# Performance work log

Hardware: AMD Instinct MI355X
Metric: run time of the kernel (lower is better)

The kernel has to match this reference:

```python
import jax, jax.numpy as jnp
import numpy as np

N_DYADIC = 0  # dyadic refinement order n (init kwarg)


def _solve_pde(inc):
    """Solve the signature-kernel Goursat PDE by finite differences.

    inc: (A, Mi, Ni) inner products <dx_i, dy_j> on the (refined) grid.
    Recurrence on grid K of shape (Mi+1, Ni+1):
      K[0,:] = K[:,0] = 1
      K[i,j] = K[i,j-1] + K[i-1,j] + K[i-1,j-1] * (inc[i-1,j-1] - 1)
    Implemented as an anti-diagonal wavefront (vectorized over batch and
    along each diagonal) so there is no O(M*N) sequential loop.
    Returns K[:, -1, -1], shape (A,).
    """
    A, Mi, Ni = inc.shape
    P = Mi + 1                      # number of grid rows
    ivec = jnp.arange(P)            # row index along a diagonal
    n_diags = Mi + Ni + 1           # diagonals d = i + j in [0, Mi+Ni]

    def step(carry, d):
        prev, prev2 = carry         # diagonals d-1 and d-2, shape (A, P)
        j = d - ivec                # column index for each row on diag d
        inc_d = inc[:, jnp.clip(ivec - 1, 0, Mi - 1),
                       jnp.clip(j - 1, 0, Ni - 1)]          # (A, P)
        # K[i,j-1] = prev[i]; K[i-1,j] = prev[i-1]; K[i-1,j-1] = prev2[i-1]
        interior = prev + jnp.roll(prev, 1, axis=1) \
                 + jnp.roll(prev2, 1, axis=1) * (inc_d - 1.0)
        in_grid = (j >= 0) & (j <= Ni)
        boundary = (ivec == 0) | (j == 0)
        new = jnp.where(in_grid, jnp.where(boundary, 1.0, interior), 0.0)
        return (new, prev), None

    init = (jnp.zeros((A, P), inc.dtype), jnp.zeros((A, P), inc.dtype))
    (last, _), _ = jax.lax.scan(step, init, jnp.arange(n_diags))
    return last[:, Mi]              # K at grid point (Mi, Ni)


def _sig_kernel(X, Y, n):
    """k(x_a, y_a) for each pair in the batch, via PDE solve."""
    f = 2 ** n
    dX = X[:, 1:] - X[:, :-1]                          # (A, M-1, D)
    dY = Y[:, 1:] - Y[:, :-1]                          # (A, N-1, D)
    C = jnp.einsum('amd,and->amn', dX, dY)             # (A, M-1, N-1)
    # dyadic refinement: each coarse increment split into 2^n equal pieces
    inc = jnp.repeat(jnp.repeat(C, f, axis=1), f, axis=2) / float(f * f)
    return _solve_pde(inc)


def setup_inputs() -> dict:
    key = jax.random.key(0)
    kx, ky = jax.random.split(key)
    A, M, D = 128, 512, 16
    # small-increment random walks so the signature kernel stays bounded
    X = 0.05 * jnp.cumsum(jax.random.normal(kx, (A, M, D), dtype=jnp.float32), axis=1)
    Y = 0.05 * jnp.cumsum(jax.random.normal(ky, (A, M, D), dtype=jnp.float32), axis=1)
    return {"X": X, "Y": Y}


def reference(X, Y):
    # SigLoss: mean_a [ k(x,x) + k(y,y) - 2 k(x,y) ]
    k_xx = _sig_kernel(X, X, N_DYADIC)
    k_yy = _sig_kernel(Y, Y, N_DYADIC)
    k_xy = _sig_kernel(X, Y, N_DYADIC)
    return jnp.mean(k_xx + k_yy - 2.0 * k_xy)
```

## Files before the change

kernel.cpp:

```cpp
#include <hip/hip_runtime.h>

#define D 16

typedef short bf16x8 __attribute__((ext_vector_type(8)));
typedef float f32x16 __attribute__((ext_vector_type(16)));
typedef float v2f __attribute__((ext_vector_type(2)));

template<int CTRL, int RMASK, bool BC>
__device__ __forceinline__ float dpp_add(float x) {
    int t = __builtin_amdgcn_update_dpp(0, __float_as_int(x), CTRL, RMASK, 0xF, BC);
    return x + __int_as_float(t);
}
__device__ __forceinline__ float wave_iscan(float x) {
    x = dpp_add<0x111, 0xF, true >(x);
    x = dpp_add<0x112, 0xF, true >(x);
    x = dpp_add<0x114, 0xF, true >(x);
    x = dpp_add<0x118, 0xF, true >(x);
    x = dpp_add<0x142, 0xA, false>(x);
    x = dpp_add<0x143, 0xC, false>(x);
    return x;
}

__device__ __forceinline__ short f2bf(float f) {
    unsigned u = __float_as_uint(f);
    unsigned r = u + 0x7FFFu + ((u >> 16) & 1u);
    return (short)(r >> 16);
}

__global__ __launch_bounds__(64, 1)
void sig_pde_kernel(const float* __restrict__ X, const float* __restrict__ Y,
                    float* __restrict__ out) {
    __shared__ float sinc[32 * 512];

    const int idx  = blockIdx.x;
    const int pair = idx >> 7;
    const int a    = idx & 127;
    const float* Pp = (pair == 1) ? Y : X;
    const float* Qp = (pair == 0) ? X : Y;
    const float* prow = Pp + (size_t)a * 512 * D;
    const float* qrow = Qp + (size_t)a * 512 * D;

    const int l  = threadIdx.x;
    const int lm = l & 31;
    const int kh = l >> 5;
    const int d0 = kh * 8;
    const bool lane0 = (l == 0);

    bf16x8 Bf[16];
    #pragma unroll
    for (int n = 0; n < 16; ++n) {
        int jj = 32 * n + lm - 1;
        if (jj < 0) jj = 0;
        const float4* y1 = (const float4*)(qrow + (size_t)(jj + 1) * D + d0);
        const float4* y0 = (const float4*)(qrow + (size_t)jj * D + d0);
        float4 h1 = y1[0], h0 = y0[0], g1 = y1[1], g0 = y0[1];
        bf16x8 f;
        f[0] = f2bf(h1.x - h0.x); f[1] = f2bf(h1.y - h0.y);
        f[2] = f2bf(h1.z - h0.z); f[3] = f2bf(h1.w - h0.w);
        f[4] = f2bf(g1.x - g0.x); f[5] = f2bf(g1.y - g0.y);
        f[6] = f2bf(g1.z - g0.z); f[7] = f2bf(g1.w - g0.w);
        Bf[n] = f;
    }

    auto loadA = [&](int b) -> bf16x8 {
        int ii = 32 * b + lm - 1;
        if (ii < 0) ii = 0;
        const float4* x1 = (const float4*)(prow + (size_t)(ii + 1) * D + d0);
        const float4* x0 = (const float4*)(prow + (size_t)ii * D + d0);
        float4 h1 = x1[0], h0 = x0[0], g1 = x1[1], g0 = x0[1];
        bf16x8 f;
        f[0] = f2bf(h1.x - h0.x); f[1] = f2bf(h1.y - h0.y);
        f[2] = f2bf(h1.z - h0.z); f[3] = f2bf(h1.w - h0.w);
        f[4] = f2bf(g1.x - g0.x); f[5] = f2bf(g1.y - g0.y);
        f[6] = f2bf(g1.z - g0.z); f[7] = f2bf(g1.w - g0.w);
        return f;
    };

    const int rot = (l >> 2) & 7;
    float* wbase = sinc + kh * 2048;

    int ea4[8];
    #pragma unroll
    for (int m = 0; m < 8; ++m) ea4[m] = (8 * l + ((m + rot) & 7)) * 4;

    float s[8];
    #pragma unroll
    for (int m = 0; m < 8; ++m) s[m] = 0.0f;
    float B = 1.0f;

    v2f ghA[8], ghB[8];
    float eA[8], eB[8];

    const f32x16 accC = {-1.f,-1.f,-1.f,-1.f,-1.f,-1.f,-1.f,-1.f,
                         -1.f,-1.f,-1.f,-1.f,-1.f,-1.f,-1.f,-1.f};

#define PREF(BUF, RB) do {                                                    \
        const char* pb_ = (const char*)sinc + (RB);                           \
        _Pragma("unroll")                                                     \
        for (int m_ = 0; m_ < 8; ++m_)                                        \
            BUF[m_] = *(const float*)(pb_ + ea4[m_]);                         \
    } while (0)

#define TOUCH(BUF) do { float tt_ = BUF[7];                                   \
        asm volatile("" : "+v"(tt_)); BUF[7] = tt_; } while (0)

#define GHBUILD(GH, E) do {                                                   \
        float p0_ = E[0] + 1.0f;  p0_ = lane0 ? 0.0f : p0_;                   \
        float c0_ = lane0 ? 0.0f : s[0];                                      \
        GH[0][0] = p0_; GH[0][1] = c0_;                                       \
        _Pragma("unroll")                                                     \
        for (int m_ = 1; m_ < 8; ++m_) {                                      \
            v2f pc_;                                                          \
            pc_[0] = E[m_] + 1.0f;                                            \
            pc_[1] = fmaf(s[m_ - 1], E[m_], s[m_]);                          \
            GH[m_] = GH[m_ - 1] + pc_;                                        \
        }                                                                     \
    } while (0)

#define SFMA(GH) do {                                                         \
        _Pragma("unroll")                                                     \
        for (int m_ = 0; m_ < 8; ++m_)                                        \
            s[m_] = fmaf(B, GH[m_][0], GH[m_][1]);                            \
    } while (0)

#define STEPROW(GHC, EP, RP, EN, GHN) do {                                    \
        TOUCH(EN);                                                            \
        SFMA(GHC);                                                            \
        float S_ = s[7];                                                      \
        float W_ = wave_iscan(S_);                      \
        PREF(EP, RP);                                     \
        GHBUILD(GHN, EN);                     \
        B = 1.0f + (W_ - S_);                                                 \
    } while (0)

#define TAILROW(GHC) do {                                                     \
        SFMA(GHC);                                                            \
        float S_ = s[7];                                                      \
        float W_ = wave_iscan(S_);                                            \
        B = 1.0f + (W_ - S_);                                                 \
    } while (0)

    bf16x8 Acur = loadA(0);

    for (int b = 0; b < 16; ++b) {
        #pragma unroll
        for (int n = 0; n < 16; ++n) {
            f32x16 acc = __builtin_amdgcn_mfma_f32_32x32x16_bf16(Acur, Bf[n], accC, 0, 0, 0);
            float* p = wbase + 32 * n + (lm & ~7) + (((l & 7) + n) & 7);
            #pragma unroll
            for (int r = 0; r < 16; ++r)
                p[(r & 3) * 512 + (r >> 2) * 4096] = acc[r];
        }
        if (b < 15) Acur = loadA(b + 1);

        if (b == 0) {
            #pragma unroll
            for (int m = 0; m < 8; ++m) { ghA[m][0] = 0.0f; ghA[m][1] = 0.0f; }
            PREF(eB, 2048);
        } else {
            PREF(eA, 0);
            PREF(eB, 2048);
            GHBUILD(ghA, eA);
        }
        for (int i = 0; i < 15; ++i) {
            const int rp1 = (2 * i + 2) * 2048;
            const int rp2 = (2 * i + 3) * 2048;
            STEPROW(ghA, eA, rp1, eB, ghB);
            STEPROW(ghB, eB, rp2, eA, ghA);
        }
        STEPROW(ghA, eA, 31 * 2048, eB, ghB);
        TAILROW(ghB);
    }

#undef TAILROW
#undef STEPROW
#undef SFMA
#undef GHBUILD
#undef TOUCH
#undef PREF

    if (l == 63) out[idx] = B + s[7];
}

__global__ void sig_reduce_kernel(const float* __restrict__ ws,
                                  float* __restrict__ out) {
    const int a = threadIdx.x;
    float v = ws[a] + ws[128 + a] - 2.0f * ws[256 + a];
    #pragma unroll
    for (int off = 32; off >= 1; off >>= 1) v += __shfl_down(v, off, 64);
    __shared__ float partial[2];
    if ((a & 63) == 0) partial[a >> 6] = v;
    __syncthreads();
    if (a == 0) out[0] = (partial[0] + partial[1]) * (1.0f / 128.0f);
}

extern "C" void kernel_launch(void* const* d_in, const int* in_sizes, int n_in,
                              void* d_out, int out_size, void* d_ws, size_t ws_size,
                              hipStream_t stream) {
    const float* X = (const float*)d_in[0];
    const float* Y = (const float*)d_in[1];
    float* out = (float*)d_out;
    float* ws  = (float*)d_ws;

    sig_pde_kernel<<<dim3(384), dim3(64), 0, stream>>>(X, Y, ws);
    sig_reduce_kernel<<<dim3(1), dim3(128), 0, stream>>>(ws, out);
}
```

Baseline: 93.19 us.

## Interleave two PDE problems per wavefront and split GEMM/scan into half-tiles

Each workgroup now solves two batch pairs at once. Their MFMA increment tiles and wavefront scan steps are interleaved, so the two independent DPP scan and FMA chains can hide each other's latency. The 32-row LDS tile is split into two 16-row halves per problem, alternating GEMM and scan phases. The grid is halved to 192 blocks, which lowers CU-level parallelism and raises register pressure in exchange for more instruction-level parallelism inside each wave.

Result: slower. 200.2 us (+114.8%).

```diff
diff --git a/kernel.cpp b/kernel.cpp
--- a/kernel.cpp
+++ b/kernel.cpp
@@ -5,21 +5,6 @@
 typedef short bf16x8 __attribute__((ext_vector_type(8)));
 typedef float f32x16 __attribute__((ext_vector_type(16)));
 typedef float v2f __attribute__((ext_vector_type(2)));
-
-template<int CTRL, int RMASK, bool BC>
-__device__ __forceinline__ float dpp_add(float x) {
-    int t = __builtin_amdgcn_update_dpp(0, __float_as_int(x), CTRL, RMASK, 0xF, BC);
-    return x + __int_as_float(t);
-}
-__device__ __forceinline__ float wave_iscan(float x) {
-    x = dpp_add<0x111, 0xF, true >(x);
-    x = dpp_add<0x112, 0xF, true >(x);
-    x = dpp_add<0x114, 0xF, true >(x);
-    x = dpp_add<0x118, 0xF, true >(x);
-    x = dpp_add<0x142, 0xA, false>(x);
-    x = dpp_add<0x143, 0xC, false>(x);
-    return x;
-}
 
 __device__ __forceinline__ short f2bf(float f) {
     unsigned u = __float_as_uint(f);
@@ -30,39 +15,60 @@
 __global__ __launch_bounds__(64, 1)
 void sig_pde_kernel(const float* __restrict__ X, const float* __restrict__ Y,
                     float* __restrict__ out) {
-    __shared__ float sinc[32 * 512];
-
-    const int idx  = blockIdx.x;
-    const int pair = idx >> 7;
-    const int a    = idx & 127;
-    const float* Pp = (pair == 1) ? Y : X;
-    const float* Qp = (pair == 0) ? X : Y;
-    const float* prow = Pp + (size_t)a * 512 * D;
-    const float* qrow = Qp + (size_t)a * 512 * D;
+    __shared__ float sinc[2 * 16 * 512];
+
+    const int bid  = blockIdx.x;
+    const int idx0 = 2 * bid;
+    const int idx1 = idx0 + 1;
+
+    const int pair0 = idx0 >> 7, a0 = idx0 & 127;
+    const int pair1 = idx1 >> 7, a1 = idx1 & 127;
+    const float* prow0 = ((pair0 == 1) ? Y : X) + (size_t)a0 * 512 * D;
+    const float* qrow0 = ((pair0 == 0) ? X : Y) + (size_t)a0 * 512 * D;
+    const float* prow1 = ((pair1 == 1) ? Y : X) + (size_t)a1 * 512 * D;
+    const float* qrow1 = ((pair1 == 0) ? X : Y) + (size_t)a1 * 512 * D;
+
+    float* lds0 = sinc;
+    float* lds1 = sinc + 16 * 512;
 
     const int l  = threadIdx.x;
     const int lm = l & 31;
     const int kh = l >> 5;
     const int d0 = kh * 8;
+    const int l7 = l & 7;
     const bool lane0 = (l == 0);
-
-    bf16x8 Bf[16];
+    const int rot = (l >> 2) & 7;
+
+    bf16x8 Bf0[16], Bf1[16];
     #pragma unroll
     for (int n = 0; n < 16; ++n) {
         int jj = 32 * n + lm - 1;
         if (jj < 0) jj = 0;
-        const float4* y1 = (const float4*)(qrow + (size_t)(jj + 1) * D + d0);
-        const float4* y0 = (const float4*)(qrow + (size_t)jj * D + d0);
-        float4 h1 = y1[0], h0 = y0[0], g1 = y1[1], g0 = y0[1];
-        bf16x8 f;
-        f[0] = f2bf(h1.x - h0.x); f[1] = f2bf(h1.y - h0.y);
-        f[2] = f2bf(h1.z - h0.z); f[3] = f2bf(h1.w - h0.w);
-        f[4] = f2bf(g1.x - g0.x); f[5] = f2bf(g1.y - g0.y);
-        f[6] = f2bf(g1.z - g0.z); f[7] = f2bf(g1.w - g0.w);
-        Bf[n] = f;
+        {
+            const float4* y1 = (const float4*)(qrow0 + (size_t)(jj + 1) * D + d0);
+            const float4* y0 = (const float4*)(qrow0 + (size_t)jj * D + d0);
+            float4 h1 = y1[0], h0 = y0[0], g1 = y1[1], g0 = y0[1];
+            bf16x8 f;
+            f[0] = f2bf(h1.x - h0.x); f[1] = f2bf(h1.y - h0.y);
+            f[2] = f2bf(h1.z - h0.z); f[3] = f2bf(h1.w - h0.w);
+            f[4] = f2bf(g1.x - g0.x); f[5] = f2bf(g1.y - g0.y);
+            f[6] = f2bf(g1.z - g0.z); f[7] = f2bf(g1.w - g0.w);
+            Bf0[n] = f;
+        }
+        {
+            const float4* y1 = (const float4*)(qrow1 + (size_t)(jj + 1) * D + d0);
+            const float4* y0 = (const float4*)(qrow1 + (size_t)jj * D + d0);
+            float4 h1 = y1[0], h0 = y0[0], g1 = y1[1], g0 = y0[1];
+            bf16x8 f;
+            f[0] = f2bf(h1.x - h0.x); f[1] = f2bf(h1.y - h0.y);
+            f[2] = f2bf(h1.z - h0.z); f[3] = f2bf(h1.w - h0.w);
+            f[4] = f2bf(g1.x - g0.x); f[5] = f2bf(g1.y - g0.y);
+            f[6] = f2bf(g1.z - g0.z); f[7] = f2bf(g1.w - g0.w);
+            Bf1[n] = f;
+        }
     }
 
-    auto loadA = [&](int b) -> bf16x8 {
+    auto loadA = [&](const float* prow, int b) -> bf16x8 {
         int ii = 32 * b + lm - 1;
         if (ii < 0) ii = 0;
         const float4* x1 = (const float4*)(prow + (size_t)(ii + 1) * D + d0);
@@ -76,26 +82,25 @@
         return f;
     };
 
-    const int rot = (l >> 2) & 7;
-    float* wbase = sinc + kh * 2048;
-
     int ea4[8];
     #pragma unroll
     for (int m = 0; m < 8; ++m) ea4[m] = (8 * l + ((m + rot) & 7)) * 4;
 
-    float s[8];
-    #pragma unroll
-    for (int m = 0; m < 8; ++m) s[m] = 0.0f;
-    float B = 1.0f;
-
-    v2f ghA[8], ghB[8];
-    float eA[8], eB[8];
+    float* wb0 = lds0 + kh * 2048 + (lm & ~7);
+    float* wb1 = lds1 + kh * 2048 + (lm & ~7);
+
+    float s0[8], s1[8];
+    #pragma unroll
+    for (int m = 0; m < 8; ++m) { s0[m] = 0.0f; s1[m] = 0.0f; }
+    float B0 = 1.0f, B1 = 1.0f;
+    v2f gh0[8], gh1[8];
+    float eA0[8], eB0[8], eA1[8], eB1[8];
 
     const f32x16 accC = {-1.f,-1.f,-1.f,-1.f,-1.f,-1.f,-1.f,-1.f,
                          -1.f,-1.f,-1.f,-1.f,-1.f,-1.f,-1.f,-1.f};
 
-#define PREF(BUF, RB) do {                                                    \
-        const char* pb_ = (const char*)sinc + (RB);                           \
+#define PREF1(BUF, LDSP, RB) do {                                             \
+        const char* pb_ = (const char*)(LDSP) + (RB);                         \
         _Pragma("unroll")                                                     \
         for (int m_ = 0; m_ < 8; ++m_)                                        \
             BUF[m_] = *(const float*)(pb_ + ea4[m_]);                         \
@@ -104,82 +109,117 @@
 #define TOUCH(BUF) do { float tt_ = BUF[7];                                   \
         asm volatile("" : "+v"(tt_)); BUF[7] = tt_; } while (0)
 
-#define GHBUILD(GH, E) do {                                                   \
-        float p0_ = E[0] + 1.0f;  p0_ = lane0 ? 0.0f : p0_;                   \
-        float c0_ = lane0 ? 0.0f : s[0];                                      \
-        GH[0][0] = p0_; GH[0][1] = c0_;                                       \
+#define GHBUILD1(GH, S, E) do {                                               \
+        float gp_ = E[0] + 1.0f;  gp_ = lane0 ? 0.0f : gp_;                   \
+        float gc_ = lane0 ? 0.0f : S[0];                                      \
+        GH[0][0] = gp_; GH[0][1] = gc_;                                       \
         _Pragma("unroll")                                                     \
         for (int m_ = 1; m_ < 8; ++m_) {                                      \
             v2f pc_;                                                          \
             pc_[0] = E[m_] + 1.0f;                                            \
-            pc_[1] = fmaf(s[m_ - 1], E[m_], s[m_]);                          \
+            pc_[1] = fmaf(S[m_ - 1], E[m_], S[m_]);                          \
             GH[m_] = GH[m_ - 1] + pc_;                                        \
         }                                                                     \
     } while (0)
 
-#define SFMA(GH) do {                                                         \
+#define SFMA1(S, BB, GH) do {                                                 \
         _Pragma("unroll")                                                     \
         for (int m_ = 0; m_ < 8; ++m_)                                        \
-            s[m_] = fmaf(B, GH[m_][0], GH[m_][1]);                            \
-    } while (0)
-
-#define STEPROW(GHC, EP, RP, EN, GHN) do {                                    \
-        TOUCH(EN);                                                            \
-        SFMA(GHC);                                                            \
-        float S_ = s[7];                                                      \
-        float W_ = wave_iscan(S_);                      \
-        PREF(EP, RP);                                     \
-        GHBUILD(GHN, EN);                     \
-        B = 1.0f + (W_ - S_);                                                 \
-    } while (0)
-
-#define TAILROW(GHC) do {                                                     \
-        SFMA(GHC);                                                            \
-        float S_ = s[7];                                                      \
-        float W_ = wave_iscan(S_);                                            \
-        B = 1.0f + (W_ - S_);                                                 \
-    } while (0)
-
-    bf16x8 Acur = loadA(0);
-
-    for (int b = 0; b < 16; ++b) {
-        #pragma unroll
-        for (int n = 0; n < 16; ++n) {
-            f32x16 acc = __builtin_amdgcn_mfma_f32_32x32x16_bf16(Acur, Bf[n], accC, 0, 0, 0);
-            float* p = wbase + 32 * n + (lm & ~7) + (((l & 7) + n) & 7);
-            #pragma unroll
-            for (int r = 0; r < 16; ++r)
-                p[(r & 3) * 512 + (r >> 2) * 4096] = acc[r];
-        }
-        if (b < 15) Acur = loadA(b + 1);
-
-        if (b == 0) {
-            #pragma unroll
-            for (int m = 0; m < 8; ++m) { ghA[m][0] = 0.0f; ghA[m][1] = 0.0f; }
-            PREF(eB, 2048);
-        } else {
-            PREF(eA, 0);
-            PREF(eB, 2048);
-            GHBUILD(ghA, eA);
-        }
-        for (int i = 0; i < 15; ++i) {
-            const int rp1 = (2 * i + 2) * 2048;
-            const int rp2 = (2 * i + 3) * 2048;
-            STEPROW(ghA, eA, rp1, eB, ghB);
-            STEPROW(ghB, eB, rp2, eA, ghA);
-        }
-        STEPROW(ghA, eA, 31 * 2048, eB, ghB);
-        TAILROW(ghB);
+            S[m_] = fmaf(BB, GH[m_][0], GH[m_][1]);                           \
+    } while (0)
+
+#define DPP2(X0, X1, CTRL, RM, BC) do {                                       \
+        int u0_ = __builtin_amdgcn_update_dpp(0, __float_as_int(X0), CTRL, RM, 0xF, BC); \
+        int u1_ = __builtin_amdgcn_update_dpp(0, __float_as_int(X1), CTRL, RM, 0xF, BC); \
+        X0 += __int_as_float(u0_); X1 += __int_as_float(u1_);                 \
+    } while (0)
+
+#define ISCAN2(X0, X1) do {                                                   \
+        DPP2(X0, X1, 0x111, 0xF, true);                                       \
+        DPP2(X0, X1, 0x112, 0xF, true);                                       \
+        DPP2(X0, X1, 0x114, 0xF, true);                                       \
+        DPP2(X0, X1, 0x118, 0xF, true);                                       \
+        DPP2(X0, X1, 0x142, 0xA, false);                                      \
+        DPP2(X0, X1, 0x143, 0xC, false);                                      \
+    } while (0)
+
+#define STEPROW2(EN0, EN1, EP0, EP1, RP) do {                                 \
+        TOUCH(EN0); TOUCH(EN1);                                               \
+        SFMA1(s0, B0, gh0); SFMA1(s1, B1, gh1);                               \
+        float S0_ = s0[7], S1_ = s1[7];                                       \
+        float W0_ = S0_, W1_ = S1_;                                           \
+        ISCAN2(W0_, W1_);                                                     \
+        PREF1(EP0, lds0, RP); PREF1(EP1, lds1, RP);                           \
+        GHBUILD1(gh0, s0, EN0); GHBUILD1(gh1, s1, EN1);                       \
+        B0 = 1.0f + (W0_ - S0_); B1 = 1.0f + (W1_ - S1_);                     \
+    } while (0)
+
+#define TAILROW2() do {                                                       \
+        SFMA1(s0, B0, gh0); SFMA1(s1, B1, gh1);                               \
+        float S0_ = s0[7], S1_ = s1[7];                                       \
+        float W0_ = S0_, W1_ = S1_;                                           \
+        ISCAN2(W0_, W1_);                                                     \
+        B0 = 1.0f + (W0_ - S0_); B1 = 1.0f + (W1_ - S1_);                     \
+    } while (0)
+
+#define GEMM_PHASE(H) do {                                                    \
+        _Pragma("unroll")                                                     \
+        for (int n_ = 0; n_ < 16; ++n_) {                                     \
+            f32x16 c0_ = __builtin_amdgcn_mfma_f32_32x32x16_bf16(Acur0, Bf0[n_], accC, 0, 0, 0); \
+            f32x16 c1_ = __builtin_amdgcn_mfma_f32_32x32x16_bf16(Acur1, Bf1[n_], accC, 0, 0, 0); \
+            float* q0_ = wb0 + 32 * n_ + ((l7 + n_) & 7);                     \
+            float* q1_ = wb1 + 32 * n_ + ((l7 + n_) & 7);                     \
+            _Pragma("unroll")                                                 \
+            for (int r_ = 0; r_ < 8; ++r_) {                                  \
+                const int off_ = (r_ & 3) * 512 + (r_ >> 2) * 4096;           \
+                q0_[off_] = c0_[8 * (H) + r_];                                \
+                q1_[off_] = c1_[8 * (H) + r_];                                \
+            }                                                                 \
+        }                                                                     \
+    } while (0)
+
+#define SCAN_PHASE(R0) do {                                                   \
+        PREF1(eA0, lds0, (R0) * 2048); PREF1(eA1, lds1, (R0) * 2048);         \
+        GHBUILD1(gh0, s0, eA0); GHBUILD1(gh1, s1, eA1);                       \
+        PREF1(eB0, lds0, ((R0) + 1) * 2048); PREF1(eB1, lds1, ((R0) + 1) * 2048); \
+        _Pragma("unroll")                                                     \
+        for (int r_ = (R0); r_ <= 14; ++r_) {                                 \
+            const int rp_ = (r_ + 2 <= 15 ? r_ + 2 : 15) * 2048;              \
+            if (((r_ - (R0)) & 1) == 0) STEPROW2(eB0, eB1, eA0, eA1, rp_);    \
+            else                        STEPROW2(eA0, eA1, eB0, eB1, rp_);    \
+        }                                                                     \
+        TAILROW2();                                                           \
+    } while (0)
+
+    bf16x8 Acur0 = loadA(prow0, 0);
+    bf16x8 Acur1 = loadA(prow1, 0);
+
+    GEMM_PHASE(0);
+    SCAN_PHASE(1);
+    GEMM_PHASE(1);
+    Acur0 = loadA(prow0, 1); Acur1 = loadA(prow1, 1);
+    SCAN_PHASE(0);
+
+    for (int b = 1; b < 16; ++b) {
+        GEMM_PHASE(0);
+        SCAN_PHASE(0);
+        GEMM_PHASE(1);
+        if (b < 15) { Acur0 = loadA(prow0, b + 1); Acur1 = loadA(prow1, b + 1); }
+        SCAN_PHASE(0);
     }
 
-#undef TAILROW
-#undef STEPROW
-#undef SFMA
-#undef GHBUILD
+#undef SCAN_PHASE
+#undef GEMM_PHASE
+#undef TAILROW2
+#undef STEPROW2
+#undef ISCAN2
+#undef DPP2
+#undef SFMA1
+#undef GHBUILD1
 #undef TOUCH
-#undef PREF
-
-    if (l == 63) out[idx] = B + s[7];
+#undef PREF1
+
+    if (l == 63) { out[idx0] = B0 + s0[7]; out[idx1] = B1 + s1[7]; }
 }
 
 __global__ void sig_reduce_kernel(const float* __restrict__ ws,
@@ -202,6 +242,6 @@
     float* out = (float*)d_out;
     float* ws  = (float*)d_ws;
 
-    sig_pde_kernel<<<dim3(384), dim3(64), 0, stream>>>(X, Y, ws);
+    sig_pde_kernel<<<dim3(192), dim3(64), 0, stream>>>(X, Y, ws);
     sig_reduce_kernel<<<dim3(1), dim3(128), 0, stream>>>(ws, out);
 }
```

## Interleave two PDE problems per wave with bf16 increment precompute kernel

Applied to the files above, without the earlier changes.

Adds a prep kernel that converts path increments to bf16 in a workspace buffer. A new dual kernel then processes two batch problems per 64-thread block, interleaving their dependent scan chains (paired DPP scans) to hide latency. GEMM and scan work are split into half-tile phases so the LDS footprint stays the same while two problems are handled. The trade-off is half the blocks (192 instead of 384), an extra kernel launch, and a global round-trip for the increments. The old path is kept as a fallback when the workspace is too small.

Measured after the change: 202.1 us. +116.9%, slower.

```diff
diff --git a/kernel.cpp b/kernel.cpp
--- a/kernel.cpp
+++ b/kernel.cpp
@@ -27,9 +27,214 @@
     return (short)(r >> 16);
 }
 
+__global__ void sig_prep_kernel(const float* __restrict__ X,
+                                const float* __restrict__ Y,
+                                unsigned short* __restrict__ T) {
+    const int blk = blockIdx.x;
+    const int src = blk >> 7;
+    const int a   = blk & 127;
+    const float* P = (src ? Y : X) + (size_t)a * 512 * D;
+    unsigned short* O = T + (size_t)blk * 512 * D;
+    for (int e = threadIdx.x; e < 511 * D; e += 256)
+        O[e] = (unsigned short)f2bf(P[e + D] - P[e]);
+    if (threadIdx.x < D) O[511 * D + threadIdx.x] = 0;
+}
+
 __global__ __launch_bounds__(64, 1)
-void sig_pde_kernel(const float* __restrict__ X, const float* __restrict__ Y,
-                    float* __restrict__ out) {
+void sig_pde_dual_kernel(const unsigned short* __restrict__ T,
+                         float* __restrict__ out) {
+    __shared__ float sinc[2 * 16 * 512];
+
+    const int bid  = blockIdx.x;
+    const int idx0 = 2 * bid, idx1 = idx0 + 1;
+    const int pair0 = idx0 >> 7, a0 = idx0 & 127;
+    const int pair1 = idx1 >> 7, a1 = idx1 & 127;
+
+    const unsigned short* TX = T;
+    const unsigned short* TY = T + (size_t)128 * 512 * D;
+    const unsigned short* tp0 = ((pair0 == 1) ? TY : TX) + (size_t)a0 * 512 * D;
+    const unsigned short* tq0 = ((pair0 == 0) ? TX : TY) + (size_t)a0 * 512 * D;
+    const unsigned short* tp1 = ((pair1 == 1) ? TY : TX) + (size_t)a1 * 512 * D;
+    const unsigned short* tq1 = ((pair1 == 0) ? TX : TY) + (size_t)a1 * 512 * D;
+
+    float* lds0 = sinc;
+    float* lds1 = sinc + 16 * 512;
+
+    const int l  = threadIdx.x;
+    const int lm = l & 31;
+    const int kh = l >> 5;
+    const int l7 = l & 7;
+    const bool lane0 = (l == 0);
+    const int rot = (l >> 2) & 7;
+
+    auto loadF = [&](const unsigned short* t, int r) -> bf16x8 {
+        int ii = r; if (ii < 0) ii = 0;
+        return *(const bf16x8*)(t + (size_t)ii * D + kh * 8);
+    };
+
+    int ea4[8];
+    #pragma unroll
+    for (int m = 0; m < 8; ++m) ea4[m] = (8 * l + ((m + rot) & 7)) * 4;
+
+    float* wb0 = lds0 + kh * 2048 + (lm & ~7);
+    float* wb1 = lds1 + kh * 2048 + (lm & ~7);
+
+    float s0[8], s1[8];
+    #pragma unroll
+    for (int m = 0; m < 8; ++m) { s0[m] = 0.0f; s1[m] = 0.0f; }
+    float B0 = 1.0f, B1 = 1.0f;
+    v2f gh0[8], gh1[8];
+    float eA0[8], eB0[8], eA1[8], eB1[8];
+
+    const f32x16 accC = {-1.f,-1.f,-1.f,-1.f,-1.f,-1.f,-1.f,-1.f,
+                         -1.f,-1.f,-1.f,-1.f,-1.f,-1.f,-1.f,-1.f};
+
+#define DPREF(BUF, LDSP, RB) do {                                             \
+        const char* pb_ = (const char*)(LDSP) + (RB);                         \
+        _Pragma("unroll")                                                     \
+        for (int m_ = 0; m_ < 8; ++m_)                                        \
+            BUF[m_] = *(const float*)(pb_ + ea4[m_]);                         \
+    } while (0)
+
+#define DTOUCH(BUF) do { float tt_ = BUF[7];                                  \
+        asm volatile("" : "+v"(tt_)); BUF[7] = tt_; } while (0)
+
+#define DGH(GH, S, E) do {                                                    \
+        float gp_ = E[0] + 1.0f;  gp_ = lane0 ? 0.0f : gp_;                   \
+        float gc_ = lane0 ? 0.0f : S[0];                                      \
+        GH[0][0] = gp_; GH[0][1] = gc_;                                       \
+        _Pragma("unroll")                                                     \
+        for (int m_ = 1; m_ < 8; ++m_) {                                      \
+            v2f pc_;                                                          \
+            pc_[0] = E[m_] + 1.0f;                                            \
+            pc_[1] = fmaf(S[m_ - 1], E[m_], S[m_]);                          \
+            GH[m_] = GH[m_ - 1] + pc_;                                        \
+        }                                                                     \
+    } while (0)
+
+#define DSF(S, BB, GH) do {                                                   \
+        _Pragma("unroll")                                                     \
+        for (int m_ = 0; m_ < 8; ++m_)                                        \
+            S[m_] = fmaf(BB, GH[m_][0], GH[m_][1]);                           \
+    } while (0)
+
+#define DPP2(X0, X1, CTRL, RM, BC) do {                                       \
+        int u0_ = __builtin_amdgcn_update_dpp(0, __float_as_int(X0), CTRL, RM, 0xF, BC); \
+        int u1_ = __builtin_amdgcn_update_dpp(0, __float_as_int(X1), CTRL, RM, 0xF, BC); \
+        X0 += __int_as_float(u0_); X1 += __int_as_float(u1_);                 \
+    } while (0)
+
+#define ISCAN2(X0, X1) do {                                                   \
+        DPP2(X0, X1, 0x111, 0xF, true);                                       \
+        DPP2(X0, X1, 0x112, 0xF, true);                                       \
+        DPP2(X0, X1, 0x114, 0xF, true);                                       \
+        DPP2(X0, X1, 0x118, 0xF, true);                                       \
+        DPP2(X0, X1, 0x142, 0xA, false);                                      \
+        DPP2(X0, X1, 0x143, 0xC, false);                                      \
+    } while (0)
+
+#define DSTEP(EN0, EN1, EP0, EP1, RP) do {                                    \
+        DTOUCH(EN0); DTOUCH(EN1);                                             \
+        DSF(s0, B0, gh0); DSF(s1, B1, gh1);                                   \
+        float S0_ = s0[7], S1_ = s1[7];                                       \
+        float W0_ = S0_, W1_ = S1_;                                           \
+        ISCAN2(W0_, W1_);                                                     \
+        DPREF(EP0, lds0, RP); DPREF(EP1, lds1, RP);                           \
+        DGH(gh0, s0, EN0); DGH(gh1, s1, EN1);                                 \
+        B0 = 1.0f + (W0_ - S0_); B1 = 1.0f + (W1_ - S1_);                     \
+    } while (0)
+
+#define DTAIL() do {                                                          \
+        DSF(s0, B0, gh0); DSF(s1, B1, gh1);                                   \
+        float S0_ = s0[7], S1_ = s1[7];                                       \
+        float W0_ = S0_, W1_ = S1_;                                           \
+        ISCAN2(W0_, W1_);                                                     \
+        B0 = 1.0f + (W0_ - S0_); B1 = 1.0f + (W1_ - S1_);                     \
+    } while (0)
+
+#define GB(N_, H_, F0, F1) do {                                               \
+        f32x16 c0_ = __builtin_amdgcn_mfma_f32_32x32x16_bf16(Acur0, F0, accC, 0, 0, 0); \
+        f32x16 c1_ = __builtin_amdgcn_mfma_f32_32x32x16_bf16(Acur1, F1, accC, 0, 0, 0); \
+        if ((N_) + 4 < 16) {                                                  \
+            F0 = loadF(tq0, 32 * ((N_) + 4) + lm - 1);                        \
+            F1 = loadF(tq1, 32 * ((N_) + 4) + lm - 1);                        \
+        }                                                                     \
+        float* g0_ = wb0 + 32 * (N_) + ((l7 + (N_)) & 7);                     \
+        float* g1_ = wb1 + 32 * (N_) + ((l7 + (N_)) & 7);                     \
+        _Pragma("unroll")                                                     \
+        for (int r_ = 0; r_ < 8; ++r_) {                                      \
+            const int off_ = (r_ & 3) * 512 + (r_ >> 2) * 4096;               \
+            g0_[off_] = c0_[8 * (H_) + r_];                                   \
+            g1_[off_] = c1_[8 * (H_) + r_];                                   \
+        }                                                                     \
+    } while (0)
+
+#define GEMM_PHASE(H) do {                                                    \
+        bf16x8 qa0 = loadF(tq0, lm - 1),       qa1 = loadF(tq1, lm - 1);      \
+        bf16x8 qb0 = loadF(tq0, 32 + lm - 1),  qb1 = loadF(tq1, 32 + lm - 1); \
+        bf16x8 qc0 = loadF(tq0, 64 + lm - 1),  qc1 = loadF(tq1, 64 + lm - 1); \
+        bf16x8 qd0 = loadF(tq0, 96 + lm - 1),  qd1 = loadF(tq1, 96 + lm - 1); \
+        GB( 0, H, qa0, qa1); GB( 1, H, qb0, qb1);                             \
+        GB( 2, H, qc0, qc1); GB( 3, H, qd0, qd1);                             \
+        GB( 4, H, qa0, qa1); GB( 5, H, qb0, qb1);                             \
+        GB( 6, H, qc0, qc1); GB( 7, H, qd0, qd1);                             \
+        GB( 8, H, qa0, qa1); GB( 9, H, qb0, qb1);                             \
+        GB(10, H, qc0, qc1); GB(11, H, qd0, qd1);                             \
+        GB(12, H, qa0, qa1); GB(13, H, qb0, qb1);                             \
+        GB(14, H, qc0, qc1); GB(15, H, qd0, qd1);                             \
+    } while (0)
+
+#define SCAN_PHASE(R0) do {                                                   \
+        DPREF(eA0, lds0, (R0) * 2048); DPREF(eA1, lds1, (R0) * 2048);         \
+        DGH(gh0, s0, eA0); DGH(gh1, s1, eA1);                                 \
+        DPREF(eB0, lds0, ((R0) + 1) * 2048); DPREF(eB1, lds1, ((R0) + 1) * 2048); \
+        _Pragma("unroll")                                                     \
+        for (int r_ = (R0); r_ <= 14; ++r_) {                                 \
+            const int rp_ = (r_ + 2 <= 15 ? r_ + 2 : 15) * 2048;              \
+            if (((r_ - (R0)) & 1) == 0) DSTEP(eB0, eB1, eA0, eA1, rp_);       \
+            else                        DSTEP(eA0, eA1, eB0, eB1, rp_);       \
+        }                                                                     \
+        DTAIL();                                                              \
+    } while (0)
+
+    bf16x8 Acur0 = loadF(tp0, lm - 1);
+    bf16x8 Acur1 = loadF(tp1, lm - 1);
+
+    GEMM_PHASE(0);
+    SCAN_PHASE(1);
+    GEMM_PHASE(1);
+    Acur0 = loadF(tp0, 32 + lm - 1); Acur1 = loadF(tp1, 32 + lm - 1);
+    SCAN_PHASE(0);
+
+    for (int b = 1; b < 16; ++b) {
+        GEMM_PHASE(0);
+        SCAN_PHASE(0);
+        GEMM_PHASE(1);
+        if (b < 15) {
+            Acur0 = loadF(tp0, 32 * (b + 1) + lm - 1);
+            Acur1 = loadF(tp1, 32 * (b + 1) + lm - 1);
+        }
+        SCAN_PHASE(0);
+    }
+
+#undef SCAN_PHASE
+#undef GEMM_PHASE
+#undef GB
+#undef DTAIL
+#undef DSTEP
+#undef ISCAN2
+#undef DPP2
+#undef DSF
+#undef DGH
+#undef DTOUCH
+#undef DPREF
+
+    if (l == 63) { out[idx0] = B0 + s0[7]; out[idx1] = B1 + s1[7]; }
+}
+
+__global__ __launch_bounds__(64, 1)
+void sig_pde_single_kernel(const float* __restrict__ X, const float* __restrict__ Y,
+                           float* __restrict__ out) {
     __shared__ float sinc[32 * 512];
 
     const int idx  = blockIdx.x;
@@ -127,9 +332,9 @@
         TOUCH(EN);                                                            \
         SFMA(GHC);                                                            \
         float S_ = s[7];                                                      \
-        float W_ = wave_iscan(S_);                      \
-        PREF(EP, RP);                                     \
-        GHBUILD(GHN, EN);                     \
+        float W_ = wave_iscan(S_);                                            \
+        PREF(EP, RP);                                                         \
+        GHBUILD(GHN, EN);                                                     \
         B = 1.0f + (W_ - S_);                                                 \
     } while (0)
 
@@ -200,8 +405,17 @@
     const float* X = (const float*)d_in[0];
     const float* Y = (const float*)d_in[1];
     float* out = (float*)d_out;
-    float* ws  = (float*)d_ws;
-
-    sig_pde_kernel<<<dim3(384), dim3(64), 0, stream>>>(X, Y, ws);
-    sig_reduce_kernel<<<dim3(1), dim3(128), 0, stream>>>(ws, out);
-}
+
+    const size_t TBYTES = (size_t)2 * 128 * 512 * D * 2;
+    if (ws_size >= TBYTES + 2048) {
+        unsigned short* T = (unsigned short*)d_ws;
+        float* part = (float*)((char*)d_ws + TBYTES);
+        sig_prep_kernel<<<dim3(256), dim3(256), 0, stream>>>(X, Y, T);
+        sig_pde_dual_kernel<<<dim3(192), dim3(64), 0, stream>>>(T, part);
+        sig_reduce_kernel<<<dim3(1), dim3(128), 0, stream>>>(part, out);
+    } else {
+        float* part = (float*)d_ws;
+        sig_pde_single_kernel<<<dim3(384), dim3(64), 0, stream>>>(X, Y, part);
+        sig_reduce_kernel<<<dim3(1), dim3(128), 0, stream>>>(part, out);
+    }
+}
```

## Pack two PDE problems per wave with half-wave scans and bf16 prep pass

Applied to the files above, without the earlier changes.

Adds a prep kernel that computes the bf16 path increments once into workspace. A new PDE kernel then assigns two batch problems to each 64-lane wave, each on a 32-lane half with 16 rows per lane and a 5-step half-wave DPP scan, and interleaves the MFMA tile generation of both problems with the scan. This halves the block count and raises the serial work per lane in exchange for fewer dependent scan steps and better MFMA/scan overlap. The original kernel is kept as a fallback when the workspace is too small.

Result: slower. 157.4 us (+68.9%).

```diff
diff --git a/kernel.cpp b/kernel.cpp
--- a/kernel.cpp
+++ b/kernel.cpp
@@ -20,6 +20,14 @@
     x = dpp_add<0x143, 0xC, false>(x);
     return x;
 }
+__device__ __forceinline__ float half_iscan(float x) {
+    x = dpp_add<0x111, 0xF, true >(x);
+    x = dpp_add<0x112, 0xF, true >(x);
+    x = dpp_add<0x114, 0xF, true >(x);
+    x = dpp_add<0x118, 0xF, true >(x);
+    x = dpp_add<0x142, 0xA, false>(x);
+    return x;
+}
 
 __device__ __forceinline__ short f2bf(float f) {
     unsigned u = __float_as_uint(f);
@@ -27,9 +35,173 @@
     return (short)(r >> 16);
 }
 
+__global__ void sig_prep_kernel(const float* __restrict__ X,
+                                const float* __restrict__ Y,
+                                unsigned short* __restrict__ T) {
+    const int blk = blockIdx.x;
+    const int src = blk >> 7;
+    const int a   = blk & 127;
+    const float* P = (src ? Y : X) + (size_t)a * 512 * D;
+    unsigned short* O = T + (size_t)blk * 512 * D;
+    for (int e = threadIdx.x; e < 511 * D; e += 256)
+        O[e] = (unsigned short)f2bf(P[e + D] - P[e]);
+    if (threadIdx.x < D) O[511 * D + threadIdx.x] = 0;
+}
+
 __global__ __launch_bounds__(64, 1)
-void sig_pde_kernel(const float* __restrict__ X, const float* __restrict__ Y,
-                    float* __restrict__ out) {
+void sig_pde_half2_kernel(const unsigned short* __restrict__ T,
+                          float* __restrict__ out) {
+    __shared__ float sinc[2 * 16 * 512];
+
+    const int bid  = blockIdx.x;
+    const int idx0 = 2 * bid, idx1 = idx0 + 1;
+    const int pair0 = idx0 >> 7, a0 = idx0 & 127;
+    const int pair1 = idx1 >> 7, a1 = idx1 & 127;
+
+    const unsigned short* TX = T;
+    const unsigned short* TY = T + (size_t)128 * 512 * D;
+    const unsigned short* tp0 = ((pair0 == 1) ? TY : TX) + (size_t)a0 * 512 * D;
+    const unsigned short* tq0 = ((pair0 == 0) ? TX : TY) + (size_t)a0 * 512 * D;
+    const unsigned short* tp1 = ((pair1 == 1) ? TY : TX) + (size_t)a1 * 512 * D;
+    const unsigned short* tq1 = ((pair1 == 0) ? TX : TY) + (size_t)a1 * 512 * D;
+
+    const int l  = threadIdx.x;
+    const int lm = l & 31;
+    const int kh = l >> 5;
+    const int l7 = l & 7;
+    const int q  = l & 31;
+    const bool q0 = (q == 0);
+
+    auto loadF = [&](const unsigned short* t, int r) -> bf16x8 {
+        int ii = r < 0 ? 0 : r;
+        return *(const bf16x8*)(t + (size_t)ii * D + kh * 8);
+    };
+
+    float* wb0 = sinc + kh * 2048 + (lm & ~7);
+    float* wb1 = sinc + 8192 + kh * 2048 + (lm & ~7);
+
+    unsigned ea8[8];
+    #pragma unroll
+    for (int m = 0; m < 8; ++m)
+        ea8[m] = (unsigned)(kh * 32768 + (16 * q + ((m + (q >> 1)) & 7)) * 4);
+
+    float s[16];
+    #pragma unroll
+    for (int m = 0; m < 16; ++m) s[m] = 0.0f;
+    float B = 1.0f;
+    v2f gh[16];
+    float eA[16], eB[16];
+
+    const f32x16 accC = {-1.f,-1.f,-1.f,-1.f,-1.f,-1.f,-1.f,-1.f,
+                         -1.f,-1.f,-1.f,-1.f,-1.f,-1.f,-1.f,-1.f};
+
+#define PREF(BUF, RB) do {                                                    \
+        const char* pb_ = (const char*)sinc + (RB);                           \
+        _Pragma("unroll")                                                     \
+        for (int m_ = 0; m_ < 16; ++m_)                                       \
+            BUF[m_] = *(const float*)(pb_ + ea8[m_ & 7] + (m_ & 8) * 4);      \
+    } while (0)
+
+#define TOUCH(BUF) do { float tt_ = BUF[15];                                  \
+        asm volatile("" : "+v"(tt_)); BUF[15] = tt_; } while (0)
+
+#define GH16(E) do {                                                          \
+        float gp_ = E[0] + 1.0f;  gp_ = q0 ? 0.0f : gp_;                      \
+        float gc_ = q0 ? 0.0f : s[0];                                         \
+        gh[0][0] = gp_; gh[0][1] = gc_;                                       \
+        _Pragma("unroll")                                                     \
+        for (int m_ = 1; m_ < 16; ++m_) {                                     \
+            v2f pc_;                                                          \
+            pc_[0] = E[m_] + 1.0f;                                            \
+            pc_[1] = fmaf(s[m_ - 1], E[m_], s[m_]);                          \
+            gh[m_] = gh[m_ - 1] + pc_;                                        \
+        }                                                                     \
+    } while (0)
+
+#define SF16() do {                                                           \
+        _Pragma("unroll")                                                     \
+        for (int m_ = 0; m_ < 16; ++m_)                                       \
+            s[m_] = fmaf(B, gh[m_][0], gh[m_][1]);                            \
+    } while (0)
+
+#define DSTEP(EN, EP, RP) do {                                                \
+        TOUCH(EN);                                                            \
+        SF16();                                                               \
+        float S_ = s[15];                                                     \
+        float W_ = half_iscan(S_);                                            \
+        PREF(EP, RP);                                                         \
+        GH16(EN);                                                             \
+        B = 1.0f + (W_ - S_);                                                 \
+    } while (0)
+
+#define DTAIL() do {                                                          \
+        SF16();                                                               \
+        float S_ = s[15];                                                     \
+        float W_ = half_iscan(S_);                                            \
+        B = 1.0f + (W_ - S_);                                                 \
+    } while (0)
+
+#define SCANP(R0) do {                                                        \
+        PREF(eA, (R0) * 2048);                                                \
+        GH16(eA);                                                             \
+        PREF(eB, ((R0) + 1) * 2048);                                          \
+        _Pragma("unroll")                                                     \
+        for (int r_ = (R0); r_ <= 14; ++r_) {                                 \
+            const int rp_ = (r_ + 2 <= 15 ? r_ + 2 : 15) * 2048;              \
+            if (((r_ - (R0)) & 1) == 0) DSTEP(eB, eA, rp_);                   \
+            else                        DSTEP(eA, eB, rp_);                   \
+        }                                                                     \
+        DTAIL();                                                              \
+    } while (0)
+
+#define GEMMP(TQ, ACUR, WB, H) do {                                           \
+        bf16x8 F_[4];                                                         \
+        _Pragma("unroll")                                                     \
+        for (int n_ = 0; n_ < 4; ++n_) F_[n_] = loadF(TQ, 32 * n_ + lm - 1);  \
+        _Pragma("unroll")                                                     \
+        for (int n_ = 0; n_ < 16; ++n_) {                                     \
+            f32x16 c_ = __builtin_amdgcn_mfma_f32_32x32x16_bf16(ACUR, F_[n_ & 3], accC, 0, 0, 0); \
+            if (n_ + 4 < 16) F_[n_ & 3] = loadF(TQ, 32 * (n_ + 4) + lm - 1);  \
+            float* g_ = (WB) + 32 * n_ + ((l7 + n_) & 7);                     \
+            _Pragma("unroll")                                                 \
+            for (int r_ = 0; r_ < 8; ++r_)                                    \
+                g_[(r_ & 3) * 512 + (r_ >> 2) * 4096] = c_[8 * (H) + r_];     \
+        }                                                                     \
+    } while (0)
+
+    bf16x8 Ac0 = loadF(tp0, lm - 1);
+    bf16x8 Ac1 = loadF(tp1, lm - 1);
+
+    for (int b = 0; b < 16; ++b) {
+        GEMMP(tq0, Ac0, wb0, 0);
+        GEMMP(tq1, Ac1, wb1, 0);
+        if (b == 0) SCANP(1);
+        else        SCANP(0);
+        GEMMP(tq0, Ac0, wb0, 1);
+        GEMMP(tq1, Ac1, wb1, 1);
+        if (b < 15) {
+            Ac0 = loadF(tp0, 32 * (b + 1) + lm - 1);
+            Ac1 = loadF(tp1, 32 * (b + 1) + lm - 1);
+        }
+        SCANP(0);
+    }
+
+#undef GEMMP
+#undef SCANP
+#undef DTAIL
+#undef DSTEP
+#undef SF16
+#undef GH16
+#undef TOUCH
+#undef PREF
+
+    if (l == 31) out[idx0] = B + s[15];
+    if (l == 63) out[idx1] = B + s[15];
+}
+
+__global__ __launch_bounds__(64, 1)
+void sig_pde_single_kernel(const float* __restrict__ X, const float* __restrict__ Y,
+                           float* __restrict__ out) {
     __shared__ float sinc[32 * 512];
 
     const int idx  = blockIdx.x;
@@ -127,9 +299,9 @@
         TOUCH(EN);                                                            \
         SFMA(GHC);                                                            \
         float S_ = s[7];                                                      \
-        float W_ = wave_iscan(S_);                      \
-        PREF(EP, RP);                                     \
-        GHBUILD(GHN, EN);                     \
+        float W_ = wave_iscan(S_);                                            \
+        PREF(EP, RP);                                                         \
+        GHBUILD(GHN, EN);                                                     \
         B = 1.0f + (W_ - S_);                                                 \
     } while (0)
 
@@ -200,8 +372,17 @@
     const float* X = (const float*)d_in[0];
     const float* Y = (const float*)d_in[1];
     float* out = (float*)d_out;
-    float* ws  = (float*)d_ws;
-
-    sig_pde_kernel<<<dim3(384), dim3(64), 0, stream>>>(X, Y, ws);
-    sig_reduce_kernel<<<dim3(1), dim3(128), 0, stream>>>(ws, out);
-}
+
+    const size_t TBYTES = (size_t)2 * 128 * 512 * D * 2;
+    if (ws_size >= TBYTES + 2048) {
+        unsigned short* T = (unsigned short*)d_ws;
+        float* part = (float*)((char*)d_ws + TBYTES);
+        sig_prep_kernel<<<dim3(256), dim3(256), 0, stream>>>(X, Y, T);
+        sig_pde_half2_kernel<<<dim3(192), dim3(64), 0, stream>>>(T, part);
+        sig_reduce_kernel<<<dim3(1), dim3(128), 0, stream>>>(part, out);
+    } else {
+        float* part = (float*)d_ws;
+        sig_pde_single_kernel<<<dim3(384), dim3(64), 0, stream>>>(X, Y, part);
+        sig_reduce_kernel<<<dim3(1), dim3(128), 0, stream>>>(part, out);
+    }
+}
```
